# Kernel optimization log

Measured on AMD Instinct MI355X. Metric: run time of the kernel, lower is better.

The kernel has to match this reference:

```python
import jax, jax.numpy as jnp
import numpy as np
from jax import lax

CHUNK = 64


def setup_inputs() -> dict:
    key = jax.random.key(0)
    k1, k2, k3, k4, k5 = jax.random.split(key, 5)
    B, H, S, K, V = 2, 16, 2048, 128, 128
    q = jax.random.normal(k1, (B, H, S, K), dtype=jnp.float32)
    k = jax.random.normal(k2, (B, H, S, K), dtype=jnp.float32)
    v = jax.random.normal(k3, (B, H, S, V), dtype=jnp.float32)
    # decay gate: negative per-dim log-decay (as produced by kda_gate)
    g = -0.5 * jax.random.uniform(k4, (B, H, S, K), dtype=jnp.float32)
    beta = jax.random.uniform(k5, (B, H, S), dtype=jnp.float32)
    return {"q": q, "k": k, "v": v, "g": g, "beta": beta}


def reference(q, k, v, g, beta):
    B, H, S, K = q.shape
    V = v.shape[-1]
    L = CHUNK
    assert S % L == 0
    scale = K ** (-0.5)
    # L2 normalize q, k
    q = q / (jnp.linalg.norm(q, axis=-1, keepdims=True) + 1e-06)
    k = k / (jnp.linalg.norm(k, axis=-1, keepdims=True) + 1e-06)
    NC = S // L
    qc = q.reshape(B, H, NC, L, K)
    kc = k.reshape(B, H, NC, L, K)
    vc = v.reshape(B, H, NC, L, V)
    gc = g.reshape(B, H, NC, L, K)
    bc = beta.reshape(B, H, NC, L)

    eye = jnp.eye(L, dtype=jnp.float32)
    mask_lower = jnp.tril(jnp.ones((L, L), dtype=jnp.float32), k=-1)
    causal_mask = jnp.tril(jnp.ones((L, L), dtype=jnp.float32))

    S0 = jnp.zeros((B, H, K, V), dtype=jnp.float32)

    def process_chunk(St, chunk_inputs):
        q_c, k_c, v_c, g_c, beta_c = chunk_inputs  # [b,h,L,*]
        g_cum = jnp.cumsum(g_c, axis=-2)                      # [b,h,L,K]
        g_total = g_cum[:, :, -1, :]                           # [b,h,K]
        # relative gate exp(g_cum_j - g_cum_i) for i (rows), j (cols)
        rel = jnp.exp(g_cum[:, :, None, :, :] - g_cum[:, :, :, None, :])  # [b,h,L,L,K]
        kk_gated = jnp.einsum('bhik,bhjk,bhijk->bhij', k_c, k_c, rel)
        M = kk_gated * mask_lower
        A = eye + beta_c[..., None] * M
        diag_beta = eye * beta_c[..., None]
        T = lax.linalg.triangular_solve(A, diag_beta, left_side=True, lower=True)
        g_cum_exp = jnp.exp(g_cum)
        k_gated = k_c * g_cum_exp                              # [b,h,L,K]
        g_cum_mean = jnp.mean(g_cum, axis=-1, keepdims=True)   # [b,h,L,1]
        v_gated = v_c * jnp.exp(g_cum_mean)
        W = jnp.einsum('bhij,bhjk->bhik', T, k_gated)
        U = jnp.einsum('bhij,bhjv->bhiv', T, v_gated)
        O_inter = jnp.einsum('bhik,bhkv->bhiv', q_c, St) * jnp.exp(g_cum_mean) * scale
        WS = jnp.einsum('bhik,bhkv->bhiv', W, St)
        correction = U - WS
        qk_gated = jnp.einsum('bhik,bhjk,bhijk->bhij', q_c, k_c, rel)
        qk_masked = qk_gated * causal_mask * scale
        O_intra = jnp.einsum('bhij,bhjv->bhiv', qk_masked, correction)
        O_chunk = O_inter + O_intra
        S_new = St * jnp.exp(g_total)[..., None]
        S_new = S_new + jnp.einsum('bhik,bhiv->bhkv', k_gated, correction)
        return S_new, O_chunk

    xs = (jnp.transpose(qc, (2, 0, 1, 3, 4)),
          jnp.transpose(kc, (2, 0, 1, 3, 4)),
          jnp.transpose(vc, (2, 0, 1, 3, 4)),
          jnp.transpose(gc, (2, 0, 1, 3, 4)),
          jnp.transpose(bc, (2, 0, 1, 3)))
    final_state, outs = lax.scan(process_chunk, S0, xs)
    output = jnp.transpose(outs, (1, 2, 0, 3, 4)).reshape(B, H, S, V)
    return output.astype(q.dtype), final_state
```

## Files before the change

kernel.cpp:

```cpp
#include <hip/hip_runtime.h>
#include <math.h>

#define CDIM 128
#define LCH  64
#define NCHK 32
#define NBH  32
#define SEQ  2048
#define NCHUNKS 1024
#define SCALE 0.08838834764831845f

typedef unsigned short u16;
typedef unsigned int   u32;
typedef __attribute__((ext_vector_type(8))) short bf16x8;
typedef __attribute__((ext_vector_type(4))) float f32x4;

__device__ __forceinline__ u16 f2bf(float f) {
    u32 u; __builtin_memcpy(&u, &f, 4);
    u32 r = u + 0x7fffu + ((u >> 16) & 1u);
    return (u16)(r >> 16);
}
__device__ __forceinline__ u32 rne_bits(float x) {
    u32 u; __builtin_memcpy(&u, &x, 4);
    return u + 0x7fffu + ((u >> 16) & 1u);
}
__device__ __forceinline__ u32 pk_rne(float a, float b) {
    return (rne_bits(a) >> 16) | (rne_bits(b) & 0xffff0000u);
}
__device__ __forceinline__ void split2(float a, float b, u32& hw, u32& lw) {
    u32 u0, u1;
    __builtin_memcpy(&u0, &a, 4);
    __builtin_memcpy(&u1, &b, 4);
    const u32 h0 = u0 & 0xffff0000u, h1 = u1 & 0xffff0000u;
    hw = (h0 >> 16) | h1;
    float f0, f1;
    __builtin_memcpy(&f0, &h0, 4);
    __builtin_memcpy(&f1, &h1, 4);
    lw = pk_rne(a - f0, b - f1);
}
__device__ __forceinline__ void split8(const float* s, uint4& hi, uint4& lo) {
    u32 hw[4], lw[4];
    #pragma unroll
    for (int m = 0; m < 4; ++m) split2(s[2*m], s[2*m+1], hw[m], lw[m]);
    hi.x = hw[0]; hi.y = hw[1]; hi.z = hw[2]; hi.w = hw[3];
    lo.x = lw[0]; lo.y = lw[1]; lo.z = lw[2]; lo.w = lw[3];
}
__device__ __forceinline__ f32x4 mfma_bf(uint4 a, uint4 b, f32x4 c) {
    union { uint4 u; bf16x8 v; } A, B;
    A.u = a; B.u = b;
    return __builtin_amdgcn_mfma_f32_16x16x32_bf16(A.v, B.v, c, 0, 0, 0);
}

extern "C" __global__ __launch_bounds__(256)
void KDABlock_4475355922517_kernel(float* out, int n, float val)
{
    int stride = gridDim.x * blockDim.x;
    for (int i = blockIdx.x * blockDim.x + threadIdx.x; i < n; i += stride)
        out[i] = val;
}

extern "C" __global__ __launch_bounds__(512)
void kda_phaseA1(const float* gq, const float* gk, const float* gg, const float* gbeta,
                 u16* wkhi, u16* wqn, float* wT, float* wG, float* wegt, float* wegcm)
{
    __shared__ float arena[8704];
    __shared__ float sbeta[64];

    const int chunk = blockIdx.x;
    const int bh = chunk >> 5, tt = chunk & 31;
    const int tid = threadIdx.x;
    const int base = bh * (SEQ * CDIM) + tt * (LCH * CDIM);
    const int row = tid >> 3, part = tid & 7;

    {
        const int col = tid & 127, seg = tid >> 7;
        float acc = 0.f;
        for (int r = 0; r < 16; ++r) {
            const int i = seg * 16 + r;
            acc += gg[base + i * CDIM + col];
            arena[i * 130 + col] = acc;
        }
        __syncthreads();
        float off = 0.f;
        for (int s = 0; s < seg; ++s) off += arena[(s * 16 + 15) * 130 + col];
        __syncthreads();
        if (seg) for (int r = 0; r < 16; ++r) arena[(seg * 16 + r) * 130 + col] += off;
        if (tid < 64) sbeta[tid] = gbeta[bh * SEQ + tt * LCH + tid];
    }
    __syncthreads();

    float gc[16];
    #pragma unroll
    for (int c = 0; c < 16; ++c) gc[c] = arena[row * 130 + part * 16 + c];
    if (tid < 128) wegt[chunk * CDIM + tid] = __expf(arena[63 * 130 + tid]);
    float egr;
    {
        float s = 0.f;
        #pragma unroll
        for (int c = 0; c < 16; ++c) s += gc[c];
        s += __shfl_xor(s, 1); s += __shfl_xor(s, 2); s += __shfl_xor(s, 4);
        egr = __expf(s * (1.f / 128.f));
        if (part == 0) wegcm[chunk * LCH + row] = egr;
    }

    float khi[16], klo[16];
    {
        float ss = 0.f;
        const float* kp = gk + base + row * CDIM + part * 16;
        #pragma unroll
        for (int c = 0; c < 16; ++c) { khi[c] = kp[c]; ss += khi[c] * khi[c]; }
        ss += __shfl_xor(ss, 1); ss += __shfl_xor(ss, 2); ss += __shfl_xor(ss, 4);
        const float inv = 1.f / (sqrtf(ss) + 1e-6f);
        #pragma unroll
        for (int c = 0; c < 16; ++c) {
            const float kn = khi[c] * inv;
            khi[c] = kn * __expf(gc[c]);
            klo[c] = kn * __expf(-gc[c]);
            wkhi[chunk * 8192 + row * CDIM + part * 16 + c] = f2bf(khi[c]);
        }
    }

    float qlo[16];
    {
        float ss = 0.f;
        const float* qp = gq + base + row * CDIM + part * 16;
        #pragma unroll
        for (int c = 0; c < 16; ++c) { qlo[c] = qp[c]; ss += qlo[c] * qlo[c]; }
        ss += __shfl_xor(ss, 1); ss += __shfl_xor(ss, 2); ss += __shfl_xor(ss, 4);
        const float inv = 1.f / (sqrtf(ss) + 1e-6f);
        const float qs = SCALE * egr * inv;
        #pragma unroll
        for (int c = 0; c < 16; ++c) {
            wqn[chunk * 8192 + row * CDIM + part * 16 + c] = f2bf(qlo[c] * qs);
            qlo[c] = qlo[c] * inv * __expf(-gc[c]);
        }
    }
    __syncthreads();

    #pragma unroll
    for (int c = 0; c < 16; ++c) arena[(part * 16 + c) * 68 + row] = khi[c];
    __syncthreads();

    float rk[8], rqm[8];
    #pragma unroll
    for (int d = 0; d < 8; ++d) { rk[d] = 0.f; rqm[d] = 0.f; }
    const int j0 = part * 8;
    const int lb8 = (row & 7) << 3;
    for (int kb = 0; kb < 8; ++kb) {
        #pragma unroll
        for (int kc = 0; kc < 16; ++kc) {
            const int k2 = kb * 16 + kc;
            const float a = __shfl(klo[kc], lb8 + kb);
            const float b = __shfl(qlo[kc], lb8 + kb);
            const float* hp = &arena[k2 * 68 + j0];
            #pragma unroll
            for (int d = 0; d < 8; ++d) { rk[d] += a * hp[d]; rqm[d] += b * hp[d]; }
        }
    }
    #pragma unroll
    for (int d = 0; d < 8; ++d) rqm[d] = (j0 + d <= row) ? rqm[d] * SCALE : 0.f;
    __syncthreads();

    #pragma unroll
    for (int d = 0; d < 8; ++d) arena[row * 68 + j0 + d] = rk[d];
    __syncthreads();

    if (tid < 64) {
        const int j = tid;
        for (int i = 0; i < LCH; ++i) {
            float s0 = 0.f, s1 = 0.f, s2 = 0.f, s3 = 0.f;
            int m = 0;
            for (; m + 4 <= i; m += 4) {
                s0 += arena[i*68 + m+0] * arena[4352 + (m+0)*68 + j];
                s1 += arena[i*68 + m+1] * arena[4352 + (m+1)*68 + j];
                s2 += arena[i*68 + m+2] * arena[4352 + (m+2)*68 + j];
                s3 += arena[i*68 + m+3] * arena[4352 + (m+3)*68 + j];
            }
            for (; m < i; ++m) s0 += arena[i*68 + m] * arena[4352 + m*68 + j];
            arena[4352 + i*68 + j] = sbeta[i] * (((j == i) ? 1.f : 0.f) - ((s0+s1)+(s2+s3)));
        }
    }
    __syncthreads();

    #pragma unroll
    for (int d = 0; d < 8; ++d)
        wT[chunk * 4096 + row * 64 + j0 + d] = arena[4352 + row * 68 + j0 + d];

    {
        float g[8];
        #pragma unroll
        for (int d = 0; d < 8; ++d) g[d] = 0.f;
        for (int mb = 0; mb < 8; ++mb) {
            #pragma unroll
            for (int d = 0; d < 8; ++d) {
                const float a = __shfl(rqm[d], lb8 + mb);
                const int m = mb * 8 + d;
                const float4 t0 = *(const float4*)&arena[4352 + m * 68 + j0];
                const float4 t1 = *(const float4*)&arena[4352 + m * 68 + j0 + 4];
                g[0] += a * t0.x; g[1] += a * t0.y; g[2] += a * t0.z; g[3] += a * t0.w;
                g[4] += a * t1.x; g[5] += a * t1.y; g[6] += a * t1.z; g[7] += a * t1.w;
            }
        }
        #pragma unroll
        for (int d = 0; d < 8; ++d)
            wG[chunk * 4096 + row * 64 + j0 + d] = g[d];
    }
}

extern "C" __global__ __launch_bounds__(256)
void kda_phaseA2(u16* slot1, u16* slot2, float* wTf, float* wGf,
                 u16* wTAl, u16* wGAl, int useLo)
{
    const int chunk = blockIdx.x;
    const int tid = threadIdx.x;
    const size_t cb16 = (size_t)chunk * 8192;
    const size_t cbf  = (size_t)chunk * 4096;

    u16* slot3u = (u16*)wTf;
    u16* slot4u = (u16*)wGf;

    uint4 ka[4], qa[4];
    #pragma unroll
    for (int i = 0; i < 4; ++i) {
        const int fw = tid + 256 * i;
        const int mt = fw >> 8, ks = (fw >> 6) & 3, l = fw & 63;
        const size_t src = cb16 + (size_t)(16 * mt + (l & 15)) * 128 + 32 * ks + 8 * (l >> 4);
        ka[i] = *(const uint4*)(slot1 + src);
        qa[i] = *(const uint4*)(slot2 + src);
    }
    u32 kt[4][4];
    #pragma unroll
    for (int i = 0; i < 4; ++i) {
        const int fw = tid + 256 * i;
        const int mt = fw >> 7, ks = (fw >> 6) & 1, l = fw & 63;
        const int col = 16 * mt + (l & 15);
        const int rb = 32 * ks + 8 * (l >> 4);
        #pragma unroll
        for (int p = 0; p < 4; ++p) {
            const u16 a = slot1[cb16 + (size_t)(rb + 2 * p) * 128 + col];
            const u16 b = slot1[cb16 + (size_t)(rb + 2 * p + 1) * 128 + col];
            kt[i][p] = (u32)a | ((u32)b << 16);
        }
    }
    float tv[2][8], gv2[2][8];
    #pragma unroll
    for (int i = 0; i < 2; ++i) {
        const int fw = tid + 256 * i;
        const int mt = fw >> 7, ks = (fw >> 6) & 1, l = fw & 63;
        const size_t src = cbf + (size_t)(16 * mt + (l & 15)) * 64 + 32 * ks + 8 * (l >> 4);
        *(float4*)&tv[i][0]  = *(const float4*)(wTf + src);
        *(float4*)&tv[i][4]  = *(const float4*)(wTf + src + 4);
        *(float4*)&gv2[i][0] = *(const float4*)(wGf + src);
        *(float4*)&gv2[i][4] = *(const float4*)(wGf + src + 4);
    }
    __syncthreads();

    #pragma unroll
    for (int i = 0; i < 4; ++i) {
        const int fw = tid + 256 * i;
        uint4 kv = ka[i];
        kv.x ^= 0x80008000u; kv.y ^= 0x80008000u;
        kv.z ^= 0x80008000u; kv.w ^= 0x80008000u;
        *(uint4*)(slot1 + cb16 + (size_t)fw * 8) = kv;
        *(uint4*)(slot2 + cb16 + (size_t)fw * 8) = qa[i];
        uint4 kw;
        kw.x = kt[i][0]; kw.y = kt[i][1]; kw.z = kt[i][2]; kw.w = kt[i][3];
        *(uint4*)(slot4u + cb16 + (size_t)fw * 8) = kw;
    }
    #pragma unroll
    for (int i = 0; i < 2; ++i) {
        const int fw = tid + 256 * i;
        uint4 th, tl, gh, gl;
        split8(tv[i],  th, tl);
        split8(gv2[i], gh, gl);
        *(uint4*)(slot3u + cb16 + (size_t)fw * 8) = th;
        *(uint4*)(slot3u + cb16 + 4096 + (size_t)fw * 8) = gh;
        if (useLo) {
            *(uint4*)(wTAl + cbf + (size_t)fw * 8) = tl;
            *(uint4*)(wGAl + cbf + (size_t)fw * 8) = gl;
        }
    }
}

extern "C" __global__ __launch_bounds__(256)
void kda_phaseB(const u16* wKA, const u16* wQA, const u16* wKTA,
                const u16* wTGh, const u16* wTAl, const u16* wGAl,
                const float* wegt, const float* wegcm,
                const float* gv, float* gout, int useLo)
{
    __shared__ float sS[128 * 17];
    __shared__ float sX[64 * 17];
    __shared__ float sC[64 * 17];
    __shared__ float sEt[128];
    __shared__ float sEm[64];

    const int bh = blockIdx.x >> 3;
    const int c0 = (blockIdx.x & 7) * 16;
    const int tid = threadIdx.x;
    const int w = tid >> 6;
    const int l = tid & 63;
    const int ln = l & 15;
    const int lh = l >> 4;

    for (int e = tid; e < 128 * 17; e += 256) sS[e] = 0.f;

    float* outO = gout + (size_t)bh * (SEQ * CDIM);
    float* outS = gout + (size_t)NBH * SEQ * CDIM + (size_t)bh * (CDIM * CDIM);

    for (int t = 0; t < NCHK; ++t) {
        const size_t ch = (size_t)(bh * NCHK + t);

        uint4 kf[4], qf[4];
        const u16* pK = wKA + ch * 8192 + (size_t)w * 2048 + (size_t)l * 8;
        const u16* pQ = wQA + ch * 8192 + (size_t)w * 2048 + (size_t)l * 8;
        #pragma unroll
        for (int ks = 0; ks < 4; ++ks) {
            kf[ks] = *(const uint4*)(pK + ks * 512);
            qf[ks] = *(const uint4*)(pQ + ks * 512);
        }
        uint4 tfh[2], gfh[2], tfl[2], gfl[2];
        const size_t tb = ch * 8192 + (size_t)w * 1024 + (size_t)l * 8;
        #pragma unroll
        for (int ks = 0; ks < 2; ++ks) {
            tfh[ks] = *(const uint4*)(wTGh + tb + ks * 512);
            gfh[ks] = *(const uint4*)(wTGh + tb + 4096 + ks * 512);
        }
        if (useLo) {
            const size_t tbl = ch * 4096 + (size_t)w * 1024 + (size_t)l * 8;
            #pragma unroll
            for (int ks = 0; ks < 2; ++ks) {
                tfl[ks] = *(const uint4*)(wTAl + tbl + ks * 512);
                gfl[ks] = *(const uint4*)(wGAl + tbl + ks * 512);
            }
        }
        uint4 ktf[2][2];
        #pragma unroll
        for (int m2 = 0; m2 < 2; ++m2)
            #pragma unroll
            for (int ks = 0; ks < 2; ++ks)
                ktf[m2][ks] = *(const uint4*)(wKTA + ch * 8192
                                + (size_t)((2*w + m2) * 2 + ks) * 512 + (size_t)l * 8);
        float vg[4];
        #pragma unroll
        for (int r = 0; r < 4; ++r) {
            const int row = 16 * w + 4 * lh + r;
            vg[r] = gv[(size_t)bh * SEQ * CDIM + (size_t)(t * LCH + row) * CDIM + c0 + ln];
        }
        if (tid < 128) sEt[tid] = wegt[ch * CDIM + tid];
        else if (tid < 192) sEm[tid - 128] = wegcm[ch * LCH + (tid - 128)];
        __syncthreads();

        f32x4 accX, accO;
        #pragma unroll
        for (int r = 0; r < 4; ++r) {
            accX[r] = vg[r] * sEm[16 * w + 4 * lh + r];
            accO[r] = 0.f;
        }

        #pragma unroll
        for (int ks = 0; ks < 4; ++ks) {
            float sv[8];
            const int kb = 32 * ks + 8 * lh;
            #pragma unroll
            for (int j = 0; j < 8; ++j) sv[j] = sS[(kb + j) * 17 + ln];
            uint4 hi, lo; split8(sv, hi, lo);
            accX = mfma_bf(kf[ks], hi, accX);
            accX = mfma_bf(kf[ks], lo, accX);
            accO = mfma_bf(qf[ks], hi, accO);
            accO = mfma_bf(qf[ks], lo, accO);
        }
        #pragma unroll
        for (int r = 0; r < 4; ++r) sX[(16 * w + 4 * lh + r) * 17 + ln] = accX[r];
        __syncthreads();

        f32x4 accC = {0.f, 0.f, 0.f, 0.f};
        #pragma unroll
        for (int ks = 0; ks < 2; ++ks) {
            float xv[8];
            const int kb = 32 * ks + 8 * lh;
            #pragma unroll
            for (int j = 0; j < 8; ++j) xv[j] = sX[(kb + j) * 17 + ln];
            uint4 xh, xl; split8(xv, xh, xl);
            accC = mfma_bf(tfh[ks], xh, accC);
            accC = mfma_bf(tfh[ks], xl, accC);
            accO = mfma_bf(gfh[ks], xh, accO);
            accO = mfma_bf(gfh[ks], xl, accO);
            if (useLo) {
                accC = mfma_bf(tfl[ks], xh, accC);
                accO = mfma_bf(gfl[ks], xh, accO);
            }
        }
        #pragma unroll
        for (int r = 0; r < 4; ++r) {
            const int row = 16 * w + 4 * lh + r;
            outO[(size_t)(t * LCH + row) * CDIM + c0 + ln] = accO[r];
            sC[row * 17 + ln] = accC[r];
        }
        __syncthreads();

        uint4 csh[2], csl[2];
        #pragma unroll
        for (int ks = 0; ks < 2; ++ks) {
            float cv[8];
            const int kb = 32 * ks + 8 * lh;
            #pragma unroll
            for (int j = 0; j < 8; ++j) cv[j] = sC[(kb + j) * 17 + ln];
            split8(cv, csh[ks], csl[ks]);
        }
        #pragma unroll
        for (int m2 = 0; m2 < 2; ++m2) {
            const int mt = 2 * w + m2;
            f32x4 accS;
            #pragma unroll
            for (int r = 0; r < 4; ++r) {
                const int row = 16 * mt + 4 * lh + r;
                accS[r] = sEt[row] * sS[row * 17 + ln];
            }
            #pragma unroll
            for (int ks = 0; ks < 2; ++ks) {
                accS = mfma_bf(ktf[m2][ks], csh[ks], accS);
                accS = mfma_bf(ktf[m2][ks], csl[ks], accS);
            }
            #pragma unroll
            for (int r = 0; r < 4; ++r) {
                const int row = 16 * mt + 4 * lh + r;
                sS[row * 17 + ln] = accS[r];
            }
        }
        __syncthreads();
    }

    {
        const int col = tid & 15, rb = (tid >> 4) * 8;
        #pragma unroll
        for (int r = 0; r < 8; ++r)
            outS[(size_t)(rb + r) * CDIM + c0 + col] = sS[(rb + r) * 17 + col];
    }
}

extern "C" __attribute__((visibility("default")))
void kernel_launch(void* const* d_in, const int* in_sizes, int n_in,
                   void* d_out, int out_size, void* d_ws, size_t ws_size,
                   hipStream_t stream)
{
    (void)in_sizes; (void)n_in; (void)out_size;

    const size_t NEED1 = (size_t)NCHUNKS * (8192*2*2 + 4096*4*2)
                       + (size_t)NCHUNKS * (CDIM + LCH) * 4;
    const size_t NEED2 = NEED1 + (size_t)NCHUNKS * 4096 * 2 * 2;
    if (d_ws == 0 || ws_size < NEED1) return;
    const int useLo = (ws_size >= NEED2) ? 1 : 0;

    const float* q    = (const float*)d_in[0];
    const float* k    = (const float*)d_in[1];
    const float* v    = (const float*)d_in[2];
    const float* g    = (const float*)d_in[3];
    const float* beta = (const float*)d_in[4];
    float* out = (float*)d_out;

    u16* slot1   = (u16*)d_ws;
    u16* slot2   = slot1 + (size_t)NCHUNKS * 8192;
    float* wT    = (float*)(slot2 + (size_t)NCHUNKS * 8192);
    float* wG    = wT + (size_t)NCHUNKS * 4096;
    float* wegt  = wG + (size_t)NCHUNKS * 4096;
    float* wegcm = wegt + (size_t)NCHUNKS * CDIM;
    u16* wTAl    = (u16*)(wegcm + (size_t)NCHUNKS * LCH);
    u16* wGAl    = wTAl + (size_t)NCHUNKS * 4096;
    if (!useLo) { wTAl = slot1; wGAl = slot1; }

    kda_phaseA1<<<NCHUNKS, 512, 0, stream>>>(q, k, g, beta, slot1, slot2,
                                             wT, wG, wegt, wegcm);
    kda_phaseA2<<<NCHUNKS, 256, 0, stream>>>(slot1, slot2, wT, wG,
                                             wTAl, wGAl, useLo);
    kda_phaseB<<<NBH * 8, 256, 0, stream>>>(slot1, slot2, (u16*)wG, (u16*)wT,
                                            wTAl, wGAl, wegt, wegcm, v, out, useLo);
}
```

Measured before the change: 300.3 us.

## Use split-bf16 MFMA for KK/QK gated Gram and G products in phaseA1

Replaces the scalar shuffle-based fp32 computation of the gated K·K and Q·K matrices and the G = QK·T product in phaseA1 with bf16 MFMA instructions. Each fp32 operand is split into high and low bf16 halves, and three MFMAs per tile recover near-fp32 accuracy. Operands are staged in a larger packed shared-memory arena. The triangular solve loop also gets a vectorized float4 read. The goal is to move the O(L²K) matrix work onto the matrix cores. The cost is more shared memory, which may lower occupancy, plus a small precision loss from the three-term split.

```diff
diff --git a/kernel.cpp b/kernel.cpp
--- a/kernel.cpp
+++ b/kernel.cpp
@@ -44,6 +44,23 @@
     hi.x = hw[0]; hi.y = hw[1]; hi.z = hw[2]; hi.w = hw[3];
     lo.x = lw[0]; lo.y = lw[1]; lo.z = lw[2]; lo.w = lw[3];
 }
+__device__ __forceinline__ u32 packsplit(float x) {
+    u32 u; __builtin_memcpy(&u, &x, 4);
+    const u32 hi = u & 0xffff0000u;
+    float fh; __builtin_memcpy(&fh, &hi, 4);
+    const u32 lo = rne_bits(x - fh) & 0xffff0000u;
+    return (hi >> 16) | lo;
+}
+__device__ __forceinline__ void unpack2(const uint4 p0, const uint4 p1, uint4& hi, uint4& lo) {
+    hi.x = (p0.x & 0xffffu) | (p0.y << 16);
+    lo.x = (p0.x >> 16)     | (p0.y & 0xffff0000u);
+    hi.y = (p0.z & 0xffffu) | (p0.w << 16);
+    lo.y = (p0.z >> 16)     | (p0.w & 0xffff0000u);
+    hi.z = (p1.x & 0xffffu) | (p1.y << 16);
+    lo.z = (p1.x >> 16)     | (p1.y & 0xffff0000u);
+    hi.w = (p1.z & 0xffffu) | (p1.w << 16);
+    lo.w = (p1.z >> 16)     | (p1.w & 0xffff0000u);
+}
 __device__ __forceinline__ f32x4 mfma_bf(uint4 a, uint4 b, f32x4 c) {
     union { uint4 u; bf16x8 v; } A, B;
     A.u = a; B.u = b;
@@ -62,14 +79,20 @@
 void kda_phaseA1(const float* gq, const float* gk, const float* gg, const float* gbeta,
                  u16* wkhi, u16* wqn, float* wT, float* wG, float* wegt, float* wegcm)
 {
-    __shared__ float arena[8704];
+    __shared__ u32 U[13056];
     __shared__ float sbeta[64];
+    float* fU = (float*)U;
 
     const int chunk = blockIdx.x;
     const int bh = chunk >> 5, tt = chunk & 31;
     const int tid = threadIdx.x;
     const int base = bh * (SEQ * CDIM) + tt * (LCH * CDIM);
     const int row = tid >> 3, part = tid & 7;
+    const int j0 = part * 8;
+    const int w = tid >> 6, l = tid & 63;
+    const int ln = l & 15, lh = l >> 4;
+    const int mt = w & 3;
+    const int nt0 = (w >> 2) * 2, nt1 = nt0 + 1;
 
     {
         const int col = tid & 127, seg = tid >> 7;
@@ -77,21 +100,21 @@
         for (int r = 0; r < 16; ++r) {
             const int i = seg * 16 + r;
             acc += gg[base + i * CDIM + col];
-            arena[i * 130 + col] = acc;
+            fU[i * 130 + col] = acc;
         }
         __syncthreads();
         float off = 0.f;
-        for (int s = 0; s < seg; ++s) off += arena[(s * 16 + 15) * 130 + col];
-        __syncthreads();
-        if (seg) for (int r = 0; r < 16; ++r) arena[(seg * 16 + r) * 130 + col] += off;
+        for (int s = 0; s < seg; ++s) off += fU[(s * 16 + 15) * 130 + col];
+        __syncthreads();
+        if (seg) for (int r = 0; r < 16; ++r) fU[(seg * 16 + r) * 130 + col] += off;
         if (tid < 64) sbeta[tid] = gbeta[bh * SEQ + tt * LCH + tid];
     }
     __syncthreads();
 
     float gc[16];
     #pragma unroll
-    for (int c = 0; c < 16; ++c) gc[c] = arena[row * 130 + part * 16 + c];
-    if (tid < 128) wegt[chunk * CDIM + tid] = __expf(arena[63 * 130 + tid]);
+    for (int c = 0; c < 16; ++c) gc[c] = fU[row * 130 + part * 16 + c];
+    if (tid < 128) wegt[chunk * CDIM + tid] = __expf(fU[63 * 130 + tid]);
     float egr;
     {
         float s = 0.f;
@@ -136,32 +159,64 @@
     }
     __syncthreads();
 
-    #pragma unroll
-    for (int c = 0; c < 16; ++c) arena[(part * 16 + c) * 68 + row] = khi[c];
-    __syncthreads();
-
-    float rk[8], rqm[8];
-    #pragma unroll
-    for (int d = 0; d < 8; ++d) { rk[d] = 0.f; rqm[d] = 0.f; }
-    const int j0 = part * 8;
-    const int lb8 = (row & 7) << 3;
-    for (int kb = 0; kb < 8; ++kb) {
-        #pragma unroll
-        for (int kc = 0; kc < 16; ++kc) {
-            const int k2 = kb * 16 + kc;
-            const float a = __shfl(klo[kc], lb8 + kb);
-            const float b = __shfl(qlo[kc], lb8 + kb);
-            const float* hp = &arena[k2 * 68 + j0];
-            #pragma unroll
-            for (int d = 0; d < 8; ++d) { rk[d] += a * hp[d]; rqm[d] += b * hp[d]; }
-        }
-    }
-    #pragma unroll
-    for (int d = 0; d < 8; ++d) rqm[d] = (j0 + d <= row) ? rqm[d] * SCALE : 0.f;
-    __syncthreads();
-
-    #pragma unroll
-    for (int d = 0; d < 8; ++d) arena[row * 68 + j0 + d] = rk[d];
+    f32x4 aKK0 = {0.f,0.f,0.f,0.f}, aKK1 = {0.f,0.f,0.f,0.f};
+    f32x4 aQK0 = {0.f,0.f,0.f,0.f}, aQK1 = {0.f,0.f,0.f,0.f};
+    #pragma unroll
+    for (int h = 0; h < 2; ++h) {
+        if ((part >> 2) == h) {
+            const int cc = (part & 3) * 16;
+            uint4 v;
+            #pragma unroll
+            for (int g4 = 0; g4 < 4; ++g4) {
+                v.x = packsplit(khi[4*g4+0]); v.y = packsplit(khi[4*g4+1]);
+                v.z = packsplit(khi[4*g4+2]); v.w = packsplit(khi[4*g4+3]);
+                *(uint4*)&U[0*4352 + row*68 + cc + 4*g4] = v;
+                v.x = packsplit(klo[4*g4+0]); v.y = packsplit(klo[4*g4+1]);
+                v.z = packsplit(klo[4*g4+2]); v.w = packsplit(klo[4*g4+3]);
+                *(uint4*)&U[1*4352 + row*68 + cc + 4*g4] = v;
+                v.x = packsplit(qlo[4*g4+0]); v.y = packsplit(qlo[4*g4+1]);
+                v.z = packsplit(qlo[4*g4+2]); v.w = packsplit(qlo[4*g4+3]);
+                *(uint4*)&U[2*4352 + row*68 + cc + 4*g4] = v;
+            }
+        }
+        __syncthreads();
+        #pragma unroll
+        for (int ks2 = 0; ks2 < 2; ++ks2) {
+            const int cb = 32*ks2 + 8*lh;
+            uint4 p0, p1, aH, aL, qH, qL, bH, bL;
+            p0 = *(const uint4*)&U[1*4352 + (16*mt+ln)*68 + cb];
+            p1 = *(const uint4*)&U[1*4352 + (16*mt+ln)*68 + cb + 4];
+            unpack2(p0, p1, aH, aL);
+            p0 = *(const uint4*)&U[2*4352 + (16*mt+ln)*68 + cb];
+            p1 = *(const uint4*)&U[2*4352 + (16*mt+ln)*68 + cb + 4];
+            unpack2(p0, p1, qH, qL);
+            p0 = *(const uint4*)&U[0*4352 + (16*nt0+ln)*68 + cb];
+            p1 = *(const uint4*)&U[0*4352 + (16*nt0+ln)*68 + cb + 4];
+            unpack2(p0, p1, bH, bL);
+            aKK0 = mfma_bf(aH, bH, aKK0); aKK0 = mfma_bf(aH, bL, aKK0);
+            aKK0 = mfma_bf(aL, bH, aKK0);
+            aQK0 = mfma_bf(qH, bH, aQK0); aQK0 = mfma_bf(qH, bL, aQK0);
+            aQK0 = mfma_bf(qL, bH, aQK0);
+            p0 = *(const uint4*)&U[0*4352 + (16*nt1+ln)*68 + cb];
+            p1 = *(const uint4*)&U[0*4352 + (16*nt1+ln)*68 + cb + 4];
+            unpack2(p0, p1, bH, bL);
+            aKK1 = mfma_bf(aH, bH, aKK1); aKK1 = mfma_bf(aH, bL, aKK1);
+            aKK1 = mfma_bf(aL, bH, aKK1);
+            aQK1 = mfma_bf(qH, bH, aQK1); aQK1 = mfma_bf(qH, bL, aQK1);
+            aQK1 = mfma_bf(qL, bH, aQK1);
+        }
+        __syncthreads();
+    }
+
+    #pragma unroll
+    for (int r = 0; r < 4; ++r) {
+        const int gr = 16*mt + 4*lh + r;
+        const int gc0 = 16*nt0 + ln, gc1 = 16*nt1 + ln;
+        fU[gr*68 + gc0] = aKK0[r];
+        fU[gr*68 + gc1] = aKK1[r];
+        fU[8704 + gr*68 + gc0] = (gc0 <= gr) ? aQK0[r] * SCALE : 0.f;
+        fU[8704 + gr*68 + gc1] = (gc1 <= gr) ? aQK1[r] * SCALE : 0.f;
+    }
     __syncthreads();
 
     if (tid < 64) {
@@ -170,39 +225,50 @@
             float s0 = 0.f, s1 = 0.f, s2 = 0.f, s3 = 0.f;
             int m = 0;
             for (; m + 4 <= i; m += 4) {
-                s0 += arena[i*68 + m+0] * arena[4352 + (m+0)*68 + j];
-                s1 += arena[i*68 + m+1] * arena[4352 + (m+1)*68 + j];
-                s2 += arena[i*68 + m+2] * arena[4352 + (m+2)*68 + j];
-                s3 += arena[i*68 + m+3] * arena[4352 + (m+3)*68 + j];
-            }
-            for (; m < i; ++m) s0 += arena[i*68 + m] * arena[4352 + m*68 + j];
-            arena[4352 + i*68 + j] = sbeta[i] * (((j == i) ? 1.f : 0.f) - ((s0+s1)+(s2+s3)));
+                const float4 k4 = *(const float4*)&fU[i*68 + m];
+                s0 += k4.x * fU[4352 + (m+0)*68 + j];
+                s1 += k4.y * fU[4352 + (m+1)*68 + j];
+                s2 += k4.z * fU[4352 + (m+2)*68 + j];
+                s3 += k4.w * fU[4352 + (m+3)*68 + j];
+            }
+            for (; m < i; ++m) s0 += fU[i*68 + m] * fU[4352 + m*68 + j];
+            fU[4352 + i*68 + j] = sbeta[i] * (((j == i) ? 1.f : 0.f) - ((s0+s1)+(s2+s3)));
         }
     }
     __syncthreads();
 
     #pragma unroll
     for (int d = 0; d < 8; ++d)
-        wT[chunk * 4096 + row * 64 + j0 + d] = arena[4352 + row * 68 + j0 + d];
+        wT[chunk * 4096 + row * 64 + j0 + d] = fU[4352 + row*68 + j0 + d];
 
     {
-        float g[8];
-        #pragma unroll
-        for (int d = 0; d < 8; ++d) g[d] = 0.f;
-        for (int mb = 0; mb < 8; ++mb) {
-            #pragma unroll
-            for (int d = 0; d < 8; ++d) {
-                const float a = __shfl(rqm[d], lb8 + mb);
-                const int m = mb * 8 + d;
-                const float4 t0 = *(const float4*)&arena[4352 + m * 68 + j0];
-                const float4 t1 = *(const float4*)&arena[4352 + m * 68 + j0 + 4];
-                g[0] += a * t0.x; g[1] += a * t0.y; g[2] += a * t0.z; g[3] += a * t0.w;
-                g[4] += a * t1.x; g[5] += a * t1.y; g[6] += a * t1.z; g[7] += a * t1.w;
-            }
-        }
-        #pragma unroll
-        for (int d = 0; d < 8; ++d)
-            wG[chunk * 4096 + row * 64 + j0 + d] = g[d];
+        f32x4 aG0 = {0.f,0.f,0.f,0.f}, aG1 = {0.f,0.f,0.f,0.f};
+        #pragma unroll
+        for (int ks2 = 0; ks2 < 2; ++ks2) {
+            const int cb = 32*ks2 + 8*lh;
+            float av[8];
+            *(float4*)&av[0] = *(const float4*)&fU[8704 + (16*mt+ln)*68 + cb];
+            *(float4*)&av[4] = *(const float4*)&fU[8704 + (16*mt+ln)*68 + cb + 4];
+            uint4 ah, al; split8(av, ah, al);
+            float bv[8];
+            uint4 bh, bl;
+            #pragma unroll
+            for (int j = 0; j < 8; ++j) bv[j] = fU[4352 + (cb+j)*68 + 16*nt0+ln];
+            split8(bv, bh, bl);
+            aG0 = mfma_bf(ah, bh, aG0); aG0 = mfma_bf(ah, bl, aG0);
+            aG0 = mfma_bf(al, bh, aG0);
+            #pragma unroll
+            for (int j = 0; j < 8; ++j) bv[j] = fU[4352 + (cb+j)*68 + 16*nt1+ln];
+            split8(bv, bh, bl);
+            aG1 = mfma_bf(ah, bh, aG1); aG1 = mfma_bf(ah, bl, aG1);
+            aG1 = mfma_bf(al, bh, aG1);
+        }
+        #pragma unroll
+        for (int r = 0; r < 4; ++r) {
+            const int gr = 16*mt + 4*lh + r;
+            wG[chunk * 4096 + gr * 64 + 16*nt0 + ln] = aG0[r];
+            wG[chunk * 4096 + gr * 64 + 16*nt1 + ln] = aG1[r];
+        }
     }
 }
 
```

Result: faster. 264.5 us (-11.9%).
